# Kernel optimization log

Measured on AMD Instinct MI355X. Metric: run time of the kernel, lower is better.

## Reference

```python
import jax, jax.numpy as jnp
from jax import lax
import numpy as np

V, H = 512, 512


def gru_cell(x, h, Wih, Whh, bih, bhh):
    # PyTorch GRUCell: r,z,n gate order
    gi = x @ Wih.T + bih
    gh = h @ Whh.T + bhh
    ir, iz, inn = jnp.split(gi, 3, axis=-1)
    hr, hz, hn = jnp.split(gh, 3, axis=-1)
    r = jax.nn.sigmoid(ir + hr)
    z = jax.nn.sigmoid(iz + hz)
    n = jnp.tanh(inn + r * hn)
    return (1.0 - z) * n + z * h


def setup_inputs() -> dict:
    key = jax.random.key(0)
    ks = jax.random.split(key, 20)
    S, T, B = 200, 200, 256
    w = lambda k, shape: (jax.random.normal(k, shape, jnp.float32) * 0.05)
    inp = {
        "input_seq": jax.random.randint(ks[0], (S, B), 0, V),
        "input_len": jax.random.randint(ks[1], (B,), 1, S + 1),
        "target_seq": jax.random.randint(ks[2], (T, B), 0, V),
        "enc_embed": w(ks[3], (V, H)),
        "enc_Wih": w(ks[4], (3 * H, H)),
        "enc_Whh": w(ks[5], (3 * H, H)),
        "enc_bih": w(ks[6], (3 * H,)),
        "enc_bhh": w(ks[7], (3 * H,)),
        "att_W": w(ks[8], (H, H)),
        "att_b": w(ks[9], (H,)),
        "dec_embed": w(ks[10], (V, H)),
        "dec_Wih": w(ks[11], (3 * H, H)),
        "dec_Whh": w(ks[12], (3 * H, H)),
        "dec_bih": w(ks[13], (3 * H,)),
        "dec_bhh": w(ks[14], (3 * H,)),
        "mlp_W": w(ks[15], (H, 2 * H)),
        "mlp_b": w(ks[16], (H,)),
        "out_W": w(ks[17], (V, H)),
        "out_b": w(ks[18], (V,)),
    }
    return inp


def reference(input_seq, input_len, target_seq, enc_embed, enc_Wih, enc_Whh,
              enc_bih, enc_bhh, att_W, att_b, dec_embed, dec_Wih, dec_Whh,
              dec_bih, dec_bhh, mlp_W, mlp_b, out_W, out_b):
    S, B = input_seq.shape
    T = target_seq.shape[0]

    # ---- Encoder: length-masked GRU (equivalent to pack/pad) ----
    xs = enc_embed[input_seq]                              # (S,B,H)
    mask = jnp.arange(S)[:, None] < input_len[None, :]     # (S,B)
    h0 = jnp.zeros((B, H), xs.dtype)

    def estep(h, inp):
        x, m = inp
        m = m[:, None]
        hn = gru_cell(x, h, enc_Wih, enc_Whh, enc_bih, enc_bhh)
        h = jnp.where(m, hn, h)
        return h, jnp.where(m, h, 0.0)                     # padded outputs are zero

    h_enc, enc_out = lax.scan(estep, h0, (xs, mask))       # h_enc (B,H), enc_out (S,B,H)

    # ---- Decoder: teacher forcing (training path) ----
    dec_tokens = jnp.concatenate(
        [jnp.ones((1, B), target_seq.dtype), target_seq[:-1]], axis=0)  # start token 1
    dec_emb = dec_embed[dec_tokens]                        # (T,B,H)

    def dstep(h, emb_t):
        ah = jax.nn.relu(h @ att_W.T + att_b)              # (B,H)
        e = jnp.einsum('sbh,bh->bs', enc_out, ah)          # additive-style score
        att = jax.nn.softmax(e, axis=1)                    # (B,S)
        ctx = jnp.einsum('sbh,bs->bh', enc_out, att)       # (B,H)
        x = jnp.tanh(jnp.concatenate([emb_t, ctx], axis=1) @ mlp_W.T + mlp_b)
        hn = gru_cell(x, h, dec_Wih, dec_Whh, dec_bih, dec_bhh)
        dist = jax.nn.softmax(hn @ out_W.T + out_b, axis=1)
        return hn, dist

    _, dists = lax.scan(dstep, h_enc, dec_emb)             # (T,B,V)

    # ---- Loss: -log p[target] with clamp (== cal_loss) ----
    p = jnp.maximum(dists, 1e-10)
    tgt_p = jnp.take_along_axis(p, target_seq[:, :, None], axis=2)[..., 0]
    loss = jnp.mean(-jnp.log(tgt_p))

    # ---- Accuracy ----
    inference = jnp.argmax(dists, axis=-1)                 # (T,B)
    temacc = (inference == target_seq).astype(jnp.float32)
    all_acc = jnp.mean(temacc)
    acc = jnp.mean((jnp.sum(1.0 - temacc, axis=0) == 0).astype(jnp.float32))
    return inference.astype(jnp.float32), loss, acc, all_acc
```

## Files before the change

### kernel.cpp

```cpp
#include <hip/hip_runtime.h>
#include <math.h>

#define B 256
#define Hh 512
#define S 200
#define T 200
#define VOC 512
#define G3 1536
#define PAD 36

struct d4 { double x, y, z, w; };
__device__ __forceinline__ d4 tod4(const float4 a) {
    d4 r; r.x = a.x; r.y = a.y; r.z = a.z; r.w = a.w; return r;
}
__device__ __forceinline__ double dotd(const d4& a, const d4& b) {
    return a.x * b.x + a.y * b.y + a.z * b.z + a.w * b.w;
}
__device__ __forceinline__ double sigd(double x) { return 1.0 / (1.0 + exp(-x)); }

__global__ __launch_bounds__(256) void gemm_at(
    const float* __restrict__ A,
    const float* __restrict__ W, int ldw, int woff,
    const float* __restrict__ bias,
    const float* __restrict__ tab, const int* __restrict__ tseq, int t,
    float* __restrict__ C, int ldc, int act)
{
    __shared__ float As[32][PAD];
    __shared__ float Ws[32][PAD];
    const int tid = threadIdx.x;
    const int tx = tid & 15, ty = tid >> 4;
    const int j0 = blockIdx.x * 32, m0 = blockIdx.y * 32;
    const int lr = tid >> 3, lc = (tid & 7) * 4;

    double acc00 = 0.0, acc01 = 0.0, acc10 = 0.0, acc11 = 0.0;

    for (int k0 = 0; k0 < 512; k0 += 32) {
        float4 av = *(const float4*)(A + (size_t)(m0 + lr) * 512 + k0 + lc);
        float4 wv = *(const float4*)(W + (size_t)(j0 + lr) * ldw + woff + k0 + lc);
        __syncthreads();
        *(float4*)&As[lr][lc] = av;
        *(float4*)&Ws[lr][lc] = wv;
        __syncthreads();
#pragma unroll
        for (int kk = 0; kk < 32; kk += 4) {
            d4 a0 = tod4(*(const float4*)&As[ty][kk]);
            d4 a1 = tod4(*(const float4*)&As[ty + 16][kk]);
            d4 b0 = tod4(*(const float4*)&Ws[tx][kk]);
            d4 b1 = tod4(*(const float4*)&Ws[tx + 16][kk]);
            acc00 += dotd(a0, b0);
            acc01 += dotd(a0, b1);
            acc10 += dotd(a1, b0);
            acc11 += dotd(a1, b1);
        }
    }

    const int ms[2] = { m0 + ty, m0 + ty + 16 };
    const int js[2] = { j0 + tx, j0 + tx + 16 };
    double accs[2][2] = { { acc00, acc01 }, { acc10, acc11 } };
#pragma unroll
    for (int mi = 0; mi < 2; ++mi) {
#pragma unroll
        for (int ji = 0; ji < 2; ++ji) {
            int m = ms[mi], j = js[ji];
            double v = accs[mi][ji];
            if (bias) v += (double)bias[j];
            if (tab) {
                int tok = (t == 0) ? 1 : tseq[(t - 1) * B + m];
                v += (double)tab[(size_t)tok * 512 + j];
            }
            if (act == 1) v = v > 0.0 ? v : 0.0;
            else if (act == 2) v = tanh(v);
            C[(size_t)m * ldc + j] = (float)v;
        }
    }
}

__global__ __launch_bounds__(256) void enc_step(
    const float* __restrict__ h_in, float* __restrict__ h_out,
    const float* __restrict__ gi_tab, const int* __restrict__ iseq,
    const int* __restrict__ ilen, const float* __restrict__ Whh,
    const float* __restrict__ bhh, int s, float* __restrict__ enc_out)
{
    __shared__ float Hs[32][PAD];
    __shared__ float Ws[48][PAD];
    const int tid = threadIdx.x;
    const int tx = tid & 15, ty = tid >> 4;
    const int j0 = blockIdx.x * 16, b0 = blockIdx.y * 32;
    const int lr = tid >> 3, lc = (tid & 7) * 4;

    double ar0 = 0.0, az0 = 0.0, an0 = 0.0;
    double ar1 = 0.0, az1 = 0.0, an1 = 0.0;

    for (int k0 = 0; k0 < 512; k0 += 32) {
        float4 hv = *(const float4*)(h_in + (size_t)(b0 + lr) * 512 + k0 + lc);
        int g0 = lr >> 4, jj0 = lr & 15;
        float4 wv0 = *(const float4*)(Whh + (size_t)(g0 * 512 + j0 + jj0) * 512 + k0 + lc);
        float4 wv1;
        if (tid < 128) {
            int jj1 = lr & 15;
            wv1 = *(const float4*)(Whh + (size_t)(2 * 512 + j0 + jj1) * 512 + k0 + lc);
        }
        __syncthreads();
        *(float4*)&Hs[lr][lc] = hv;
        *(float4*)&Ws[lr][lc] = wv0;
        if (tid < 128) *(float4*)&Ws[32 + lr][lc] = wv1;
        __syncthreads();
#pragma unroll
        for (int kk = 0; kk < 32; kk += 4) {
            d4 a0 = tod4(*(const float4*)&Hs[ty][kk]);
            d4 a1 = tod4(*(const float4*)&Hs[ty + 16][kk]);
            d4 wr = tod4(*(const float4*)&Ws[tx][kk]);
            d4 wz = tod4(*(const float4*)&Ws[16 + tx][kk]);
            d4 wn = tod4(*(const float4*)&Ws[32 + tx][kk]);
            ar0 += dotd(a0, wr); az0 += dotd(a0, wz); an0 += dotd(a0, wn);
            ar1 += dotd(a1, wr); az1 += dotd(a1, wz); an1 += dotd(a1, wn);
        }
    }

    const int j = j0 + tx;
    const double br = (double)bhh[j], bz = (double)bhh[512 + j], bn = (double)bhh[1024 + j];
    double gr[2] = { ar0, ar1 }, gz[2] = { az0, az1 }, gn[2] = { an0, an1 };
#pragma unroll
    for (int bb = 0; bb < 2; ++bb) {
        int b = b0 + ty + 16 * bb;
        int tok = iseq[s * B + b];
        const float* gi = gi_tab + (size_t)tok * G3;
        double r = sigd((double)gi[j] + gr[bb] + br);
        double z = sigd((double)gi[512 + j] + gz[bb] + bz);
        double n = tanh((double)gi[1024 + j] + r * (gn[bb] + bn));
        float hold = h_in[(size_t)b * 512 + j];
        float hn = (float)((1.0 - z) * n + z * (double)hold);
        bool msk = s < ilen[b];
        float hnew = msk ? hn : hold;
        h_out[(size_t)b * 512 + j] = hnew;
        enc_out[((size_t)s * B + b) * 512 + j] = msk ? hnew : 0.f;
    }
}

__global__ __launch_bounds__(256) void dec_gru(
    const float* __restrict__ x, const float* __restrict__ h_in,
    const float* __restrict__ Wih, const float* __restrict__ Whh,
    const float* __restrict__ bih, const float* __restrict__ bhh,
    float* __restrict__ h_out)
{
    __shared__ float Xs[32][PAD];
    __shared__ float Hs[32][PAD];
    __shared__ float Wi[48][PAD];
    __shared__ float Wh[48][PAD];
    const int tid = threadIdx.x;
    const int tx = tid & 15, ty = tid >> 4;
    const int j0 = blockIdx.x * 16, b0 = blockIdx.y * 32;
    const int lr = tid >> 3, lc = (tid & 7) * 4;

    double air0 = 0, aiz0 = 0, ain0 = 0, ahr0 = 0, ahz0 = 0, ahn0 = 0;
    double air1 = 0, aiz1 = 0, ain1 = 0, ahr1 = 0, ahz1 = 0, ahn1 = 0;

    for (int k0 = 0; k0 < 512; k0 += 32) {
        float4 xv = *(const float4*)(x + (size_t)(b0 + lr) * 512 + k0 + lc);
        float4 hv = *(const float4*)(h_in + (size_t)(b0 + lr) * 512 + k0 + lc);
        int g0 = lr >> 4, jj0 = lr & 15;
        float4 wi0 = *(const float4*)(Wih + (size_t)(g0 * 512 + j0 + jj0) * 512 + k0 + lc);
        float4 wh0 = *(const float4*)(Whh + (size_t)(g0 * 512 + j0 + jj0) * 512 + k0 + lc);
        float4 wi1, wh1;
        if (tid < 128) {
            int jj1 = lr & 15;
            wi1 = *(const float4*)(Wih + (size_t)(2 * 512 + j0 + jj1) * 512 + k0 + lc);
            wh1 = *(const float4*)(Whh + (size_t)(2 * 512 + j0 + jj1) * 512 + k0 + lc);
        }
        __syncthreads();
        *(float4*)&Xs[lr][lc] = xv;
        *(float4*)&Hs[lr][lc] = hv;
        *(float4*)&Wi[lr][lc] = wi0;
        *(float4*)&Wh[lr][lc] = wh0;
        if (tid < 128) { *(float4*)&Wi[32 + lr][lc] = wi1; *(float4*)&Wh[32 + lr][lc] = wh1; }
        __syncthreads();
#pragma unroll
        for (int kk = 0; kk < 32; kk += 4) {
            d4 x0 = tod4(*(const float4*)&Xs[ty][kk]);
            d4 x1 = tod4(*(const float4*)&Xs[ty + 16][kk]);
            d4 h0 = tod4(*(const float4*)&Hs[ty][kk]);
            d4 h1 = tod4(*(const float4*)&Hs[ty + 16][kk]);
            d4 wir = tod4(*(const float4*)&Wi[tx][kk]);
            d4 wiz = tod4(*(const float4*)&Wi[16 + tx][kk]);
            d4 win = tod4(*(const float4*)&Wi[32 + tx][kk]);
            d4 whr = tod4(*(const float4*)&Wh[tx][kk]);
            d4 whz = tod4(*(const float4*)&Wh[16 + tx][kk]);
            d4 whn = tod4(*(const float4*)&Wh[32 + tx][kk]);
            air0 += dotd(x0, wir); aiz0 += dotd(x0, wiz); ain0 += dotd(x0, win);
            ahr0 += dotd(h0, whr); ahz0 += dotd(h0, whz); ahn0 += dotd(h0, whn);
            air1 += dotd(x1, wir); aiz1 += dotd(x1, wiz); ain1 += dotd(x1, win);
            ahr1 += dotd(h1, whr); ahz1 += dotd(h1, whz); ahn1 += dotd(h1, whn);
        }
    }

    const int j = j0 + tx;
    const double bir = (double)bih[j], biz = (double)bih[512 + j], bin = (double)bih[1024 + j];
    const double bhr = (double)bhh[j], bhz = (double)bhh[512 + j], bhn = (double)bhh[1024 + j];
    double ir[2] = { air0, air1 }, iz[2] = { aiz0, aiz1 }, in_[2] = { ain0, ain1 };
    double hr[2] = { ahr0, ahr1 }, hz[2] = { ahz0, ahz1 }, hn_[2] = { ahn0, ahn1 };
#pragma unroll
    for (int bb = 0; bb < 2; ++bb) {
        int b = b0 + ty + 16 * bb;
        double r = sigd(ir[bb] + bir + hr[bb] + bhr);
        double z = sigd(iz[bb] + biz + hz[bb] + bhz);
        double n = tanh(in_[bb] + bin + r * (hn_[bb] + bhn));
        float hold = h_in[(size_t)b * 512 + j];
        h_out[(size_t)b * 512 + j] = (float)((1.0 - z) * n + z * (double)hold);
    }
}

__global__ __launch_bounds__(256) void attn_step(
    const float* __restrict__ enc_out, const float* __restrict__ ah,
    float* __restrict__ ctx)
{
    const int b = blockIdx.x;
    const int tid = threadIdx.x;
    const int wave = tid >> 6, lane = tid & 63;

    const d4 a1 = tod4(*(const float4*)(ah + (size_t)b * 512 + lane * 4));
    const d4 a2 = tod4(*(const float4*)(ah + (size_t)b * 512 + 256 + lane * 4));

    double m = -INFINITY, l = 0.0;
    d4 c1 = { 0, 0, 0, 0 }, c2 = { 0, 0, 0, 0 };

    for (int s = wave; s < S; s += 4) {
        const float* row = enc_out + ((size_t)s * B + b) * 512;
        d4 e1 = tod4(*(const float4*)(row + lane * 4));
        d4 e2 = tod4(*(const float4*)(row + 256 + lane * 4));
        double p = dotd(e1, a1) + dotd(e2, a2);
#pragma unroll
        for (int off = 32; off >= 1; off >>= 1) p += __shfl_xor(p, off, 64);
        double mn = fmax(m, p);
        double sc = exp(m - mn);
        double w = exp(p - mn);
        l = l * sc + w;
        c1.x = c1.x * sc + w * e1.x; c1.y = c1.y * sc + w * e1.y;
        c1.z = c1.z * sc + w * e1.z; c1.w = c1.w * sc + w * e1.w;
        c2.x = c2.x * sc + w * e2.x; c2.y = c2.y * sc + w * e2.y;
        c2.z = c2.z * sc + w * e2.z; c2.w = c2.w * sc + w * e2.w;
        m = mn;
    }

    __shared__ double sm[4], sl[4];
    __shared__ double scx[4][512];
    if (lane == 0) { sm[wave] = m; sl[wave] = l; }
    scx[wave][lane * 4 + 0] = c1.x; scx[wave][lane * 4 + 1] = c1.y;
    scx[wave][lane * 4 + 2] = c1.z; scx[wave][lane * 4 + 3] = c1.w;
    scx[wave][256 + lane * 4 + 0] = c2.x; scx[wave][256 + lane * 4 + 1] = c2.y;
    scx[wave][256 + lane * 4 + 2] = c2.z; scx[wave][256 + lane * 4 + 3] = c2.w;
    __syncthreads();

    double M = fmax(fmax(sm[0], sm[1]), fmax(sm[2], sm[3]));
    double w0 = exp(sm[0] - M), w1 = exp(sm[1] - M);
    double w2 = exp(sm[2] - M), w3 = exp(sm[3] - M);
    double L = sl[0] * w0 + sl[1] * w1 + sl[2] * w2 + sl[3] * w3;

    for (int j = tid; j < 512; j += 256) {
        double v = scx[0][j] * w0 + scx[1][j] * w1 + scx[2][j] * w2 + scx[3][j] * w3;
        ctx[(size_t)b * 512 + j] = (float)(v / L);
    }
}

__global__ __launch_bounds__(256) void softmax_loss(
    const float* __restrict__ logits, const int* __restrict__ target,
    int t, float* __restrict__ nll, float* __restrict__ inference)
{
    const int b = blockIdx.x, tid = threadIdx.x;
    const float l0 = logits[(size_t)b * 512 + tid];
    const float l1 = logits[(size_t)b * 512 + 256 + tid];

    __shared__ float sv[256];
    sv[tid] = fmaxf(l0, l1);
    __syncthreads();
    for (int off = 128; off > 0; off >>= 1) {
        if (tid < off) sv[tid] = fmaxf(sv[tid], sv[tid + off]);
        __syncthreads();
    }
    const double mx = (double)sv[0];
    __syncthreads();

    __shared__ double sd[256];
    const double e0 = exp((double)l0 - mx);
    const double e1 = exp((double)l1 - mx);
    sd[tid] = e0 + e1;
    __syncthreads();
    for (int off = 128; off > 0; off >>= 1) {
        if (tid < off) sd[tid] += sd[tid + off];
        __syncthreads();
    }
    const double Z = sd[0];
    __syncthreads();

    const float p0 = (float)(e0 / Z);
    const float p1 = (float)(e1 / Z);
    float v; int idx;
    if (p0 >= p1) { v = p0; idx = tid; } else { v = p1; idx = 256 + tid; }

    __shared__ float pv[256];
    __shared__ int pi[256];
    pv[tid] = v; pi[tid] = idx;
    __syncthreads();
    for (int off = 128; off > 0; off >>= 1) {
        if (tid < off) {
            float ov = pv[tid + off]; int oi = pi[tid + off];
            if (ov > pv[tid] || (ov == pv[tid] && oi < pi[tid])) { pv[tid] = ov; pi[tid] = oi; }
        }
        __syncthreads();
    }

    if (tid == 0) {
        int tgt = target[t * B + b];
        float pt = (float)(exp((double)logits[(size_t)b * 512 + tgt] - mx) / Z);
        pt = fmaxf(pt, 1e-10f);
        nll[t * B + b] = (float)(-log((double)pt));
        inference[t * B + b] = (float)pi[0];
    }
}

__global__ __launch_bounds__(256) void finalize_k(
    const float* __restrict__ nll, const float* __restrict__ inference,
    const int* __restrict__ target, float* __restrict__ out3)
{
    const int tid = threadIdx.x;
    int wrong = 0;
    double match = 0.0;
    const int b = tid;
    for (int t = 0; t < T; ++t) {
        float inf = inference[t * B + b];
        float tg = (float)target[t * B + b];
        bool ok = (inf == tg);
        match += ok ? 1.0 : 0.0;
        wrong |= !ok;
    }
    double lsum = 0.0;
    for (int i = tid; i < T * B; i += 256) lsum += (double)nll[i];

    __shared__ double sl[256], sm_[256], sa[256];
    sl[tid] = lsum; sm_[tid] = match; sa[tid] = wrong ? 0.0 : 1.0;
    __syncthreads();
    for (int off = 128; off > 0; off >>= 1) {
        if (tid < off) {
            sl[tid] += sl[tid + off];
            sm_[tid] += sm_[tid + off];
            sa[tid] += sa[tid + off];
        }
        __syncthreads();
    }
    if (tid == 0) {
        out3[0] = (float)(sl[0] / (double)(T * B));
        out3[1] = (float)(sa[0] / (double)B);
        out3[2] = (float)(sm_[0] / (double)(T * B));
    }
}

extern "C" void kernel_launch(void* const* d_in, const int* in_sizes, int n_in,
                              void* d_out, int out_size, void* d_ws, size_t ws_size,
                              hipStream_t stream)
{
    const int*   input_seq  = (const int*)d_in[0];
    const int*   input_len  = (const int*)d_in[1];
    const int*   target_seq = (const int*)d_in[2];
    const float* enc_embed  = (const float*)d_in[3];
    const float* enc_Wih    = (const float*)d_in[4];
    const float* enc_Whh    = (const float*)d_in[5];
    const float* enc_bih    = (const float*)d_in[6];
    const float* enc_bhh    = (const float*)d_in[7];
    const float* att_W      = (const float*)d_in[8];
    const float* att_b      = (const float*)d_in[9];
    const float* dec_embed  = (const float*)d_in[10];
    const float* dec_Wih    = (const float*)d_in[11];
    const float* dec_Whh    = (const float*)d_in[12];
    const float* dec_bih    = (const float*)d_in[13];
    const float* dec_bhh    = (const float*)d_in[14];
    const float* mlp_W      = (const float*)d_in[15];
    const float* mlp_b      = (const float*)d_in[16];
    const float* out_W      = (const float*)d_in[17];
    const float* out_b      = (const float*)d_in[18];

    float* out = (float*)d_out;

    float* gi_tab  = (float*)d_ws;
    float* mlp_tab = gi_tab + (size_t)VOC * G3;
    float* h_ping  = mlp_tab + (size_t)VOC * Hh;
    float* h_pong  = h_ping + (size_t)B * Hh;
    float* ah      = h_pong + (size_t)B * Hh;
    float* ctx     = ah + (size_t)B * Hh;
    float* xbuf    = ctx + (size_t)B * Hh;
    float* logits  = xbuf + (size_t)B * Hh;
    float* nll     = logits + (size_t)B * Hh;
    float* enc_out = nll + (size_t)T * B;

    hipMemsetAsync(h_ping, 0, (size_t)B * Hh * sizeof(float), stream);

    gemm_at<<<dim3(48, 16), 256, 0, stream>>>(
        enc_embed, enc_Wih, 512, 0, enc_bih, nullptr, nullptr, 0, gi_tab, G3, 0);
    gemm_at<<<dim3(16, 16), 256, 0, stream>>>(
        dec_embed, mlp_W, 1024, 0, mlp_b, nullptr, nullptr, 0, mlp_tab, Hh, 0);

    for (int s = 0; s < S; ++s) {
        const float* hc = (s & 1) ? h_pong : h_ping;
        float* hx = (s & 1) ? h_ping : h_pong;
        enc_step<<<dim3(32, 8), 256, 0, stream>>>(
            hc, hx, gi_tab, input_seq, input_len, enc_Whh, enc_bhh, s, enc_out);
    }

    for (int t = 0; t < T; ++t) {
        const float* hc = (t & 1) ? h_pong : h_ping;
        float* hx = (t & 1) ? h_ping : h_pong;
        gemm_at<<<dim3(16, 8), 256, 0, stream>>>(
            hc, att_W, 512, 0, att_b, nullptr, nullptr, 0, ah, Hh, 1);
        attn_step<<<dim3(B), 256, 0, stream>>>(enc_out, ah, ctx);
        gemm_at<<<dim3(16, 8), 256, 0, stream>>>(
            ctx, mlp_W, 1024, 512, nullptr, mlp_tab, target_seq, t, xbuf, Hh, 2);
        dec_gru<<<dim3(32, 8), 256, 0, stream>>>(
            xbuf, hc, dec_Wih, dec_Whh, dec_bih, dec_bhh, hx);
        gemm_at<<<dim3(16, 8), 256, 0, stream>>>(
            hx, out_W, 512, 0, out_b, nullptr, nullptr, 0, logits, Hh, 0);
        softmax_loss<<<dim3(B), 256, 0, stream>>>(logits, target_seq, t, nll, out);
    }

    finalize_k<<<dim3(1), 256, 0, stream>>>(nll, out, target_seq, out + (size_t)T * B);
}
```

Before: 33.93 ms.

## Fuse decoder step kernels, skip padded encoder work and attention rows

Restructures the decoder loop from six to three launches per step. The att_W and out_W GEMMs become one dual GEMM over the same hidden state, computing step t-1's logits alongside step t's attention projection. Attention, the ctx half of the MLP and the previous step's softmax/loss are fused into one launch, and attention iterates only over valid positions, adding the zero-padded rows' contribution analytically. Encoder tiles whose batch rows are all past their length skip the GEMM and only copy state, trading extra code complexity and a skewed per-step pipeline for fewer launches and less wasted work.

```diff
diff --git a/kernel.cpp b/kernel.cpp
--- a/kernel.cpp
+++ b/kernel.cpp
@@ -22,8 +22,7 @@
     const float* __restrict__ A,
     const float* __restrict__ W, int ldw, int woff,
     const float* __restrict__ bias,
-    const float* __restrict__ tab, const int* __restrict__ tseq, int t,
-    float* __restrict__ C, int ldc, int act)
+    float* __restrict__ C, int ldc)
 {
     __shared__ float As[32][PAD];
     __shared__ float Ws[32][PAD];
@@ -53,26 +52,16 @@
             acc11 += dotd(a1, b1);
         }
     }
-
     const int ms[2] = { m0 + ty, m0 + ty + 16 };
     const int js[2] = { j0 + tx, j0 + tx + 16 };
     double accs[2][2] = { { acc00, acc01 }, { acc10, acc11 } };
 #pragma unroll
-    for (int mi = 0; mi < 2; ++mi) {
+    for (int mi = 0; mi < 2; ++mi)
 #pragma unroll
         for (int ji = 0; ji < 2; ++ji) {
             int m = ms[mi], j = js[ji];
-            double v = accs[mi][ji];
-            if (bias) v += (double)bias[j];
-            if (tab) {
-                int tok = (t == 0) ? 1 : tseq[(t - 1) * B + m];
-                v += (double)tab[(size_t)tok * 512 + j];
-            }
-            if (act == 1) v = v > 0.0 ? v : 0.0;
-            else if (act == 2) v = tanh(v);
-            C[(size_t)m * ldc + j] = (float)v;
-        }
-    }
+            C[(size_t)m * ldc + j] = (float)(accs[mi][ji] + (double)bias[j]);
+        }
 }
 
 __global__ __launch_bounds__(256) void enc_step(
@@ -87,6 +76,19 @@
     const int tx = tid & 15, ty = tid >> 4;
     const int j0 = blockIdx.x * 16, b0 = blockIdx.y * 32;
     const int lr = tid >> 3, lc = (tid & 7) * 4;
+
+    int ml = 0;
+    for (int i = 0; i < 32; ++i) ml = max(ml, ilen[b0 + i]);
+    if (s >= ml) {
+        const int j = j0 + tx;
+#pragma unroll
+        for (int bb = 0; bb < 2; ++bb) {
+            int b = b0 + ty + 16 * bb;
+            h_out[(size_t)b * 512 + j] = h_in[(size_t)b * 512 + j];
+            enc_out[((size_t)s * B + b) * 512 + j] = 0.f;
+        }
+        return;
+    }
 
     double ar0 = 0.0, az0 = 0.0, an0 = 0.0;
     double ar1 = 0.0, az1 = 0.0, an1 = 0.0;
@@ -116,7 +118,6 @@
             ar1 += dotd(a1, wr); az1 += dotd(a1, wz); an1 += dotd(a1, wn);
         }
     }
-
     const int j = j0 + tx;
     const double br = (double)bhh[j], bz = (double)bhh[512 + j], bn = (double)bhh[1024 + j];
     double gr[2] = { ar0, ar1 }, gz[2] = { az0, az1 }, gn[2] = { an0, an1 };
@@ -134,6 +135,185 @@
         float hnew = msk ? hn : hold;
         h_out[(size_t)b * 512 + j] = hnew;
         enc_out[((size_t)s * B + b) * 512 + j] = msk ? hnew : 0.f;
+    }
+}
+
+__global__ __launch_bounds__(256) void gemm_dual(
+    const float* __restrict__ h,
+    const float* __restrict__ att_W, const float* __restrict__ att_b,
+    const float* __restrict__ out_W, const float* __restrict__ out_b,
+    float* __restrict__ ah, float* __restrict__ logits)
+{
+    __shared__ float As[32][PAD];
+    __shared__ float Ws[32][PAD];
+    const int tid = threadIdx.x;
+    const int tx = tid & 15, ty = tid >> 4;
+    const int j0 = blockIdx.x * 32, m0 = blockIdx.y * 32;
+    const int lr = tid >> 3, lc = (tid & 7) * 4;
+    const bool is_att = (j0 < 512);
+
+    double acc00 = 0.0, acc01 = 0.0, acc10 = 0.0, acc11 = 0.0;
+
+    for (int k0 = 0; k0 < 512; k0 += 32) {
+        float4 av = *(const float4*)(h + (size_t)(m0 + lr) * 512 + k0 + lc);
+        int R = j0 + lr;
+        const float* wsrc = is_att ? (att_W + (size_t)R * 512)
+                                   : (out_W + (size_t)(R - 512) * 512);
+        float4 wv = *(const float4*)(wsrc + k0 + lc);
+        __syncthreads();
+        *(float4*)&As[lr][lc] = av;
+        *(float4*)&Ws[lr][lc] = wv;
+        __syncthreads();
+#pragma unroll
+        for (int kk = 0; kk < 32; kk += 4) {
+            d4 a0 = tod4(*(const float4*)&As[ty][kk]);
+            d4 a1 = tod4(*(const float4*)&As[ty + 16][kk]);
+            d4 b0 = tod4(*(const float4*)&Ws[tx][kk]);
+            d4 b1 = tod4(*(const float4*)&Ws[tx + 16][kk]);
+            acc00 += dotd(a0, b0);
+            acc01 += dotd(a0, b1);
+            acc10 += dotd(a1, b0);
+            acc11 += dotd(a1, b1);
+        }
+    }
+    const int ms[2] = { m0 + ty, m0 + ty + 16 };
+    const int js[2] = { j0 + tx, j0 + tx + 16 };
+    double accs[2][2] = { { acc00, acc01 }, { acc10, acc11 } };
+#pragma unroll
+    for (int mi = 0; mi < 2; ++mi)
+#pragma unroll
+        for (int ji = 0; ji < 2; ++ji) {
+            int m = ms[mi], R = js[ji];
+            double v = accs[mi][ji];
+            if (is_att) {
+                v += (double)att_b[R];
+                if (v < 0.0) v = 0.0;
+                ah[(size_t)m * 512 + R] = (float)v;
+            } else {
+                v += (double)out_b[R - 512];
+                logits[(size_t)m * 512 + (R - 512)] = (float)v;
+            }
+        }
+}
+
+__global__ __launch_bounds__(256) void attn_x_softmax(
+    const float* __restrict__ enc_out, const float* __restrict__ ah,
+    const float* __restrict__ mlp_W, const float* __restrict__ mlp_tab,
+    const int* __restrict__ input_len, const int* __restrict__ target_seq,
+    const float* __restrict__ logits, int t,
+    float* __restrict__ xbuf, float* __restrict__ nll,
+    float* __restrict__ inference)
+{
+    const int bid = blockIdx.x, tid = threadIdx.x;
+
+    if (bid < B) {
+        if (t >= T) return;
+        __shared__ float scx[4][512];
+        __shared__ double sml[8];
+        __shared__ float ctxl[512];
+        const int b = bid;
+        const int wave = tid >> 6, lane = tid & 63;
+        const int len = input_len[b];
+        const float* ahb = ah + (size_t)b * 512;
+        d4 aa1 = tod4(*(const float4*)(ahb + lane * 4));
+        d4 aa2 = tod4(*(const float4*)(ahb + 256 + lane * 4));
+        double m = -INFINITY, l = 0.0;
+        d4 c1 = {0,0,0,0}, c2 = {0,0,0,0};
+        for (int s = wave; s < len; s += 4) {
+            const float* row = enc_out + ((size_t)s * B + b) * 512;
+            d4 e1 = tod4(*(const float4*)(row + lane * 4));
+            d4 e2 = tod4(*(const float4*)(row + 256 + lane * 4));
+            double p = dotd(e1, aa1) + dotd(e2, aa2);
+#pragma unroll
+            for (int off = 32; off >= 1; off >>= 1) p += __shfl_xor(p, off, 64);
+            double mn = fmax(m, p);
+            double sc = exp(m - mn), w = exp(p - mn);
+            l = l * sc + w;
+            c1.x = c1.x * sc + w * e1.x; c1.y = c1.y * sc + w * e1.y;
+            c1.z = c1.z * sc + w * e1.z; c1.w = c1.w * sc + w * e1.w;
+            c2.x = c2.x * sc + w * e2.x; c2.y = c2.y * sc + w * e2.y;
+            c2.z = c2.z * sc + w * e2.z; c2.w = c2.w * sc + w * e2.w;
+            m = mn;
+        }
+        if (lane == 0) { sml[wave] = m; sml[4 + wave] = l; }
+        *(float4*)&scx[wave][lane * 4] =
+            make_float4((float)c1.x, (float)c1.y, (float)c1.z, (float)c1.w);
+        *(float4*)&scx[wave][256 + lane * 4] =
+            make_float4((float)c2.x, (float)c2.y, (float)c2.z, (float)c2.w);
+        __syncthreads();
+        double M = fmax(fmax(sml[0], sml[1]), fmax(sml[2], sml[3]));
+        if (len < S) M = fmax(M, 0.0);
+        double w0 = exp(sml[0] - M), w1x = exp(sml[1] - M);
+        double w2x = exp(sml[2] - M), w3 = exp(sml[3] - M);
+        double L = sml[4] * w0 + sml[5] * w1x + sml[6] * w2x + sml[7] * w3
+                 + (double)(S - len) * exp(0.0 - M);
+        for (int jj = tid; jj < 512; jj += 256) {
+            double v = (double)scx[0][jj] * w0 + (double)scx[1][jj] * w1x
+                     + (double)scx[2][jj] * w2x + (double)scx[3][jj] * w3;
+            ctxl[jj] = (float)(v / L);
+        }
+        __syncthreads();
+
+        const int tok = (t == 0) ? 1 : target_seq[(t - 1) * B + b];
+        d4 cv1 = tod4(*(const float4*)&ctxl[lane * 8]);
+        d4 cv2 = tod4(*(const float4*)&ctxl[lane * 8 + 4]);
+        for (int jr = wave; jr < 512; jr += 4) {
+            const float* wr = mlp_W + (size_t)jr * 1024 + 512;
+            d4 wv1 = tod4(*(const float4*)(wr + lane * 8));
+            d4 wv2 = tod4(*(const float4*)(wr + lane * 8 + 4));
+            double p = dotd(wv1, cv1) + dotd(wv2, cv2);
+#pragma unroll
+            for (int off = 32; off >= 1; off >>= 1) p += __shfl_xor(p, off, 64);
+            if (lane == 0)
+                xbuf[(size_t)b * 512 + jr] =
+                    (float)tanh((double)mlp_tab[(size_t)tok * 512 + jr] + p);
+        }
+    } else {
+        if (t < 1) return;
+        __shared__ float red_f[256];
+        __shared__ double red_d[256];
+        __shared__ int red_i[256];
+        const int sb = bid - B;
+        const float* lg = logits + (size_t)sb * 512;
+        const float l0 = lg[tid], l1 = lg[256 + tid];
+        red_f[tid] = fmaxf(l0, l1);
+        __syncthreads();
+        for (int off = 128; off > 0; off >>= 1) {
+            if (tid < off) red_f[tid] = fmaxf(red_f[tid], red_f[tid + off]);
+            __syncthreads();
+        }
+        const double mx = (double)red_f[0];
+        __syncthreads();
+        const double e0 = exp((double)l0 - mx), e1 = exp((double)l1 - mx);
+        red_d[tid] = e0 + e1;
+        __syncthreads();
+        for (int off = 128; off > 0; off >>= 1) {
+            if (tid < off) red_d[tid] += red_d[tid + off];
+            __syncthreads();
+        }
+        const double Z = red_d[0];
+        __syncthreads();
+        const float p0 = (float)(e0 / Z), p1 = (float)(e1 / Z);
+        float v; int idx;
+        if (p0 >= p1) { v = p0; idx = tid; } else { v = p1; idx = 256 + tid; }
+        red_f[tid] = v; red_i[tid] = idx;
+        __syncthreads();
+        for (int off = 128; off > 0; off >>= 1) {
+            if (tid < off) {
+                float ov = red_f[tid + off]; int oi = red_i[tid + off];
+                if (ov > red_f[tid] || (ov == red_f[tid] && oi < red_i[tid])) {
+                    red_f[tid] = ov; red_i[tid] = oi;
+                }
+            }
+            __syncthreads();
+        }
+        if (tid == 0) {
+            int tg = target_seq[(t - 1) * B + sb];
+            float pt = (float)(exp((double)lg[tg] - mx) / Z);
+            pt = fmaxf(pt, 1e-10f);
+            nll[(t - 1) * B + sb] = (float)(-log((double)pt));
+            inference[(t - 1) * B + sb] = (float)red_i[0];
+        }
     }
 }
 
@@ -192,7 +372,6 @@
             ahr1 += dotd(h1, whr); ahz1 += dotd(h1, whz); ahn1 += dotd(h1, whn);
         }
     }
-
     const int j = j0 + tx;
     const double bir = (double)bih[j], biz = (double)bih[512 + j], bin = (double)bih[1024 + j];
     const double bhr = (double)bhh[j], bhz = (double)bhh[512 + j], bhn = (double)bhh[1024 + j];
@@ -206,114 +385,6 @@
         double n = tanh(in_[bb] + bin + r * (hn_[bb] + bhn));
         float hold = h_in[(size_t)b * 512 + j];
         h_out[(size_t)b * 512 + j] = (float)((1.0 - z) * n + z * (double)hold);
-    }
-}
-
-__global__ __launch_bounds__(256) void attn_step(
-    const float* __restrict__ enc_out, const float* __restrict__ ah,
-    float* __restrict__ ctx)
-{
-    const int b = blockIdx.x;
-    const int tid = threadIdx.x;
-    const int wave = tid >> 6, lane = tid & 63;
-
-    const d4 a1 = tod4(*(const float4*)(ah + (size_t)b * 512 + lane * 4));
-    const d4 a2 = tod4(*(const float4*)(ah + (size_t)b * 512 + 256 + lane * 4));
-
-    double m = -INFINITY, l = 0.0;
-    d4 c1 = { 0, 0, 0, 0 }, c2 = { 0, 0, 0, 0 };
-
-    for (int s = wave; s < S; s += 4) {
-        const float* row = enc_out + ((size_t)s * B + b) * 512;
-        d4 e1 = tod4(*(const float4*)(row + lane * 4));
-        d4 e2 = tod4(*(const float4*)(row + 256 + lane * 4));
-        double p = dotd(e1, a1) + dotd(e2, a2);
-#pragma unroll
-        for (int off = 32; off >= 1; off >>= 1) p += __shfl_xor(p, off, 64);
-        double mn = fmax(m, p);
-        double sc = exp(m - mn);
-        double w = exp(p - mn);
-        l = l * sc + w;
-        c1.x = c1.x * sc + w * e1.x; c1.y = c1.y * sc + w * e1.y;
-        c1.z = c1.z * sc + w * e1.z; c1.w = c1.w * sc + w * e1.w;
-        c2.x = c2.x * sc + w * e2.x; c2.y = c2.y * sc + w * e2.y;
-        c2.z = c2.z * sc + w * e2.z; c2.w = c2.w * sc + w * e2.w;
-        m = mn;
-    }
-
-    __shared__ double sm[4], sl[4];
-    __shared__ double scx[4][512];
-    if (lane == 0) { sm[wave] = m; sl[wave] = l; }
-    scx[wave][lane * 4 + 0] = c1.x; scx[wave][lane * 4 + 1] = c1.y;
-    scx[wave][lane * 4 + 2] = c1.z; scx[wave][lane * 4 + 3] = c1.w;
-    scx[wave][256 + lane * 4 + 0] = c2.x; scx[wave][256 + lane * 4 + 1] = c2.y;
-    scx[wave][256 + lane * 4 + 2] = c2.z; scx[wave][256 + lane * 4 + 3] = c2.w;
-    __syncthreads();
-
-    double M = fmax(fmax(sm[0], sm[1]), fmax(sm[2], sm[3]));
-    double w0 = exp(sm[0] - M), w1 = exp(sm[1] - M);
-    double w2 = exp(sm[2] - M), w3 = exp(sm[3] - M);
-    double L = sl[0] * w0 + sl[1] * w1 + sl[2] * w2 + sl[3] * w3;
-
-    for (int j = tid; j < 512; j += 256) {
-        double v = scx[0][j] * w0 + scx[1][j] * w1 + scx[2][j] * w2 + scx[3][j] * w3;
-        ctx[(size_t)b * 512 + j] = (float)(v / L);
-    }
-}
-
-__global__ __launch_bounds__(256) void softmax_loss(
-    const float* __restrict__ logits, const int* __restrict__ target,
-    int t, float* __restrict__ nll, float* __restrict__ inference)
-{
-    const int b = blockIdx.x, tid = threadIdx.x;
-    const float l0 = logits[(size_t)b * 512 + tid];
-    const float l1 = logits[(size_t)b * 512 + 256 + tid];
-
-    __shared__ float sv[256];
-    sv[tid] = fmaxf(l0, l1);
-    __syncthreads();
-    for (int off = 128; off > 0; off >>= 1) {
-        if (tid < off) sv[tid] = fmaxf(sv[tid], sv[tid + off]);
-        __syncthreads();
-    }
-    const double mx = (double)sv[0];
-    __syncthreads();
-
-    __shared__ double sd[256];
-    const double e0 = exp((double)l0 - mx);
-    const double e1 = exp((double)l1 - mx);
-    sd[tid] = e0 + e1;
-    __syncthreads();
-    for (int off = 128; off > 0; off >>= 1) {
-        if (tid < off) sd[tid] += sd[tid + off];
-        __syncthreads();
-    }
-    const double Z = sd[0];
-    __syncthreads();
-
-    const float p0 = (float)(e0 / Z);
-    const float p1 = (float)(e1 / Z);
-    float v; int idx;
-    if (p0 >= p1) { v = p0; idx = tid; } else { v = p1; idx = 256 + tid; }
-
-    __shared__ float pv[256];
-    __shared__ int pi[256];
-    pv[tid] = v; pi[tid] = idx;
-    __syncthreads();
-    for (int off = 128; off > 0; off >>= 1) {
-        if (tid < off) {
-            float ov = pv[tid + off]; int oi = pi[tid + off];
-            if (ov > pv[tid] || (ov == pv[tid] && oi < pi[tid])) { pv[tid] = ov; pi[tid] = oi; }
-        }
-        __syncthreads();
-    }
-
-    if (tid == 0) {
-        int tgt = target[t * B + b];
-        float pt = (float)(exp((double)logits[(size_t)b * 512 + tgt] - mx) / Z);
-        pt = fmaxf(pt, 1e-10f);
-        nll[t * B + b] = (float)(-log((double)pt));
-        inference[t * B + b] = (float)pi[0];
     }
 }
 
@@ -381,43 +452,41 @@
 
     float* gi_tab  = (float*)d_ws;
     float* mlp_tab = gi_tab + (size_t)VOC * G3;
-    float* h_ping  = mlp_tab + (size_t)VOC * Hh;
-    float* h_pong  = h_ping + (size_t)B * Hh;
-    float* ah      = h_pong + (size_t)B * Hh;
-    float* ctx     = ah + (size_t)B * Hh;
-    float* xbuf    = ctx + (size_t)B * Hh;
-    float* logits  = xbuf + (size_t)B * Hh;
-    float* nll     = logits + (size_t)B * Hh;
-    float* enc_out = nll + (size_t)T * B;
-
-    hipMemsetAsync(h_ping, 0, (size_t)B * Hh * sizeof(float), stream);
+    float* h0      = mlp_tab + (size_t)VOC * Hh;
+    float* h1      = h0 + (size_t)B * Hh;
+    float* ahb     = h1 + (size_t)B * Hh;
+    float* xb      = ahb + (size_t)B * Hh;
+    float* lgb     = xb + (size_t)B * Hh;
+    float* nllb    = lgb + (size_t)B * Hh;
+    float* enc_out = nllb + (size_t)T * B;
+
+    hipMemsetAsync(h0, 0, (size_t)B * Hh * sizeof(float), stream);
 
     gemm_at<<<dim3(48, 16), 256, 0, stream>>>(
-        enc_embed, enc_Wih, 512, 0, enc_bih, nullptr, nullptr, 0, gi_tab, G3, 0);
+        enc_embed, enc_Wih, 512, 0, enc_bih, gi_tab, G3);
     gemm_at<<<dim3(16, 16), 256, 0, stream>>>(
-        dec_embed, mlp_W, 1024, 0, mlp_b, nullptr, nullptr, 0, mlp_tab, Hh, 0);
+        dec_embed, mlp_W, 1024, 0, mlp_b, mlp_tab, Hh);
 
     for (int s = 0; s < S; ++s) {
-        const float* hc = (s & 1) ? h_pong : h_ping;
-        float* hx = (s & 1) ? h_ping : h_pong;
+        const float* hc = (s & 1) ? h1 : h0;
+        float* hx = (s & 1) ? h0 : h1;
         enc_step<<<dim3(32, 8), 256, 0, stream>>>(
             hc, hx, gi_tab, input_seq, input_len, enc_Whh, enc_bhh, s, enc_out);
     }
 
-    for (int t = 0; t < T; ++t) {
-        const float* hc = (t & 1) ? h_pong : h_ping;
-        float* hx = (t & 1) ? h_ping : h_pong;
-        gemm_at<<<dim3(16, 8), 256, 0, stream>>>(
-            hc, att_W, 512, 0, att_b, nullptr, nullptr, 0, ah, Hh, 1);
-        attn_step<<<dim3(B), 256, 0, stream>>>(enc_out, ah, ctx);
-        gemm_at<<<dim3(16, 8), 256, 0, stream>>>(
-            ctx, mlp_W, 1024, 512, nullptr, mlp_tab, target_seq, t, xbuf, Hh, 2);
-        dec_gru<<<dim3(32, 8), 256, 0, stream>>>(
-            xbuf, hc, dec_Wih, dec_Whh, dec_bih, dec_bhh, hx);
-        gemm_at<<<dim3(16, 8), 256, 0, stream>>>(
-            hx, out_W, 512, 0, out_b, nullptr, nullptr, 0, logits, Hh, 0);
-        softmax_loss<<<dim3(B), 256, 0, stream>>>(logits, target_seq, t, nll, out);
-    }
-
-    finalize_k<<<dim3(1), 256, 0, stream>>>(nll, out, target_seq, out + (size_t)T * B);
-}
+    for (int t = 0; t <= T; ++t) {
+        const float* hc = (t & 1) ? h1 : h0;
+        float* hx = (t & 1) ? h0 : h1;
+        gemm_dual<<<dim3(32, 8), 256, 0, stream>>>(
+            hc, att_W, att_b, out_W, out_b, ahb, lgb);
+        attn_x_softmax<<<dim3(2 * B), 256, 0, stream>>>(
+            enc_out, ahb, mlp_W, mlp_tab, input_len, target_seq,
+            lgb, t, xb, nllb, out);
+        if (t < T) {
+            dec_gru<<<dim3(32, 8), 256, 0, stream>>>(
+                xb, hc, dec_Wih, dec_Whh, dec_bih, dec_bhh, hx);
+        }
+    }
+
+    finalize_k<<<dim3(1), 256, 0, stream>>>(nllb, out, target_seq, out + (size_t)T * B);
+}
```

New measurement: 44.82 ms. +32.1%, slower.
